# Optimization experiments

Hardware: AMD Instinct MI355X
Metric: run time of the kernel (lower is better)

The kernel has to match this reference:

```python
import jax, jax.numpy as jnp
import numpy as np

NPOINT = 2048
RADIUS = 0.1
NSAMPLE = 32


def fps(xyz, npoint):
    # Furthest point sampling, deterministic start at index 0 (matches pointnet2_utils).
    B, N, _ = xyz.shape
    dist0 = jnp.full((B, N), 1e10, dtype=xyz.dtype)
    far0 = jnp.zeros((B,), dtype=jnp.int32)

    def step(carry, _):
        dist, far = carry
        centroid = jnp.take_along_axis(xyz, far[:, None, None], axis=1)  # (B,1,3)
        d = jnp.sum((xyz - centroid) ** 2, axis=-1)                      # (B,N)
        dist = jnp.minimum(dist, d)
        new_far = jnp.argmax(dist, axis=-1).astype(jnp.int32)
        return (dist, new_far), far

    _, idx = jax.lax.scan(step, (dist0, far0), None, length=npoint)
    return idx.T  # (B, npoint)


def ball_query(xyz, new_xyz, radius, nsample):
    # For each center, indices of up to nsample points within radius (pad with first hit).
    N = xyz.shape[1]
    sqr = jnp.sum((new_xyz[:, :, None, :] - xyz[:, None, :, :]) ** 2, axis=-1)  # (B,S,N)
    cand = jnp.where(sqr <= radius * radius, jnp.arange(N, dtype=jnp.int32), N)
    cand = jnp.sort(cand, axis=-1)[:, :, :nsample]  # (B,S,K)
    first = cand[:, :, :1]
    first = jnp.where(first == N, 0, first)
    return jnp.where(cand == N, first, cand)


def batched_gather(points, idx):
    # points (B,N,C), idx (B,...) -> (B,...,C)
    return jax.vmap(lambda p, i: p[i])(points, idx)


def reference(xyz, features, W0, b0, W1, b1, W2, b2):
    # xyz: (B,N,3), features: (B,C,N)
    fps_idx = fps(xyz, NPOINT)                                  # (B,S)
    new_xyz = batched_gather(xyz, fps_idx)                      # (B,S,3)
    idx = ball_query(xyz, new_xyz, RADIUS, NSAMPLE)             # (B,S,K)

    grouped_xyz = batched_gather(xyz, idx) - new_xyz[:, :, None, :]   # (B,S,K,3) relative coords
    grouped_feat = batched_gather(features.transpose(0, 2, 1), idx)   # (B,S,K,C)
    grouped = jnp.concatenate([grouped_xyz, grouped_feat], axis=-1)   # (B,S,K,C+3)
    x = grouped.transpose(0, 3, 1, 2)                                 # (B,C+3,S,K)

    # SharedMLP: 1x1 conv2d + ReLU stack
    x = jax.nn.relu(jnp.einsum('oi,bisk->bosk', W0, x) + b0[None, :, None, None])
    x = jax.nn.relu(jnp.einsum('oi,bisk->bosk', W1, x) + b1[None, :, None, None])
    x = jax.nn.relu(jnp.einsum('oi,bisk->bosk', W2, x) + b2[None, :, None, None])

    new_features = jnp.max(x, axis=-1)  # max-pool over nsample -> (B,128,S)
    return new_xyz, new_features


def setup_inputs() -> dict:
    key = jax.random.key(0)
    ks = jax.random.split(key, 8)
    B, N, C = 4, 8192, 64
    s = 0.05  # keep activations in a sane range through 3 relu layers
    return {
        'xyz': jax.random.uniform(ks[0], (B, N, 3), dtype=jnp.float32),
        'features': jax.random.normal(ks[1], (B, C, N), dtype=jnp.float32),
        'W0': jax.random.normal(ks[2], (64, 67), dtype=jnp.float32) * s,
        'b0': jax.random.normal(ks[3], (64,), dtype=jnp.float32) * s,
        'W1': jax.random.normal(ks[4], (64, 64), dtype=jnp.float32) * s,
        'b1': jax.random.normal(ks[5], (64,), dtype=jnp.float32) * s,
        'W2': jax.random.normal(ks[6], (128, 64), dtype=jnp.float32) * s,
        'b2': jax.random.normal(ks[7], (128,), dtype=jnp.float32) * s,
    }
```

## Files before the change

### kernel.cpp

```cpp
#include <hip/hip_runtime.h>

#define NB 4
#define NPTS 8192
#define NPOINT 2048
#define NSAMPLE 32
#define CF 64
#define CIN 67
#define G 8

typedef float f32x2 __attribute__((ext_vector_type(2)));
typedef unsigned long long u64;

__device__ __forceinline__ f32x2 pk_add(f32x2 a, f32x2 b) {
  f32x2 d;
  asm("v_pk_add_f32 %0, %1, %2" : "=v"(d) : "v"(a), "v"(b));
  return d;
}
__device__ __forceinline__ f32x2 pk_mul(f32x2 a, f32x2 b) {
  f32x2 d;
  asm("v_pk_mul_f32 %0, %1, %2" : "=v"(d) : "v"(a), "v"(b));
  return d;
}

template <int CTRL, int RM>
__device__ __forceinline__ int dppi(int v) {
  return __builtin_amdgcn_update_dpp(0, v, CTRL, RM, 0xf, true);
}
template <int CTRL, int RM>
__device__ __forceinline__ u64 kstep(u64 k) {
  unsigned lo = (unsigned)k, hi = (unsigned)(k >> 32);
  unsigned olo = (unsigned)dppi<CTRL, RM>((int)lo);
  unsigned ohi = (unsigned)dppi<CTRL, RM>((int)hi);
  u64 o = ((u64)ohi << 32) | olo;
  return o > k ? o : k;
}
__device__ __forceinline__ u64 wave_max_key(u64 key) {
  key = kstep<0x111, 0xf>(key);
  key = kstep<0x112, 0xf>(key);
  key = kstep<0x114, 0xf>(key);
  key = kstep<0x118, 0xf>(key);
  key = kstep<0x142, 0xa>(key);
  key = kstep<0x143, 0xc>(key);
  return key;
}
__device__ __forceinline__ unsigned wave_scan_incl(unsigned v) {
  v += (unsigned)__builtin_amdgcn_update_dpp(0, (int)v, 0x111, 0xf, 0xf, true);
  v += (unsigned)__builtin_amdgcn_update_dpp(0, (int)v, 0x112, 0xf, 0xf, true);
  v += (unsigned)__builtin_amdgcn_update_dpp(0, (int)v, 0x114, 0xf, 0xf, true);
  v += (unsigned)__builtin_amdgcn_update_dpp(0, (int)v, 0x118, 0xf, 0xf, true);
  v += (unsigned)__builtin_amdgcn_update_dpp(0, (int)v, 0x142, 0xa, 0xf, true);
  v += (unsigned)__builtin_amdgcn_update_dpp(0, (int)v, 0x143, 0xc, 0xf, true);
  return v;
}

__device__ __forceinline__ int cell16(float x) {
  int c = (int)(x * 16.0f);
  return c > 15 ? 15 : (c < 0 ? 0 : c);
}
__device__ __forceinline__ unsigned morton12(int ix, int iy, int iz) {
  unsigned m = 0;
#pragma unroll
  for (int k = 0; k < 4; ++k) {
    m |= ((unsigned)((ix >> k) & 1) << (3 * k + 2)) |
         ((unsigned)((iy >> k) & 1) << (3 * k + 1)) |
         ((unsigned)((iz >> k) & 1) << (3 * k + 0));
  }
  return m;
}

__global__ __launch_bounds__(512) void fps_kernel(const float* __restrict__ xyz,
                                                  float* __restrict__ new_xyz) {
  const int b = blockIdx.x;
  const int tid = threadIdx.x;
  const int lane = tid & 63;
  const int wid = tid >> 6;
  __shared__ float sx[NPTS], sy[NPTS], sz[NPTS];
  __shared__ unsigned short sidx16[NPTS];
  __shared__ unsigned offs[4096];
  __shared__ unsigned wsum[8];
  __shared__ int farhist[NPOINT];
  __shared__ __align__(16) u64 skey[2][8];

  const float* xb = xyz + (size_t)b * NPTS * 3;
  for (int i = tid; i < NPTS; i += 512) {
    sx[i] = xb[3 * i + 0];
    sy[i] = xb[3 * i + 1];
    sz[i] = xb[3 * i + 2];
  }
  for (int i = tid; i < 4096; i += 512) offs[i] = 0;
  __syncthreads();
  for (int r = 0; r < 16; ++r) {
    int i = tid + r * 512;
    atomicAdd(&offs[morton12(cell16(sx[i]), cell16(sy[i]), cell16(sz[i]))], 1u);
  }
  __syncthreads();
  unsigned loc[8];
  unsigned s = 0;
#pragma unroll
  for (int q = 0; q < 8; ++q) {
    loc[q] = s;
    s += offs[tid * 8 + q];
  }
  unsigned inc = wave_scan_incl(s);
  if (lane == 63) wsum[wid] = inc;
  __syncthreads();
  unsigned pre = 0;
#pragma unroll
  for (int w = 0; w < 8; ++w) pre += (w < wid) ? wsum[w] : 0u;
  unsigned excl = pre + inc - s;
  __syncthreads();
#pragma unroll
  for (int q = 0; q < 8; ++q) offs[tid * 8 + q] = excl + loc[q];
  __syncthreads();
  for (int r = 0; r < 16; ++r) {
    int i = tid + r * 512;
    unsigned m = morton12(cell16(sx[i]), cell16(sy[i]), cell16(sz[i]));
    unsigned pos = atomicAdd(&offs[m], 1u);
    sidx16[pos] = (unsigned short)i;
  }
  __syncthreads();

  f32x2 px[8], py[8], pz[8];
  float dist[16];
  unsigned noid[16];
  float blx = 1e30f, bhx = -1e30f, bly = 1e30f, bhy = -1e30f,
        blz = 1e30f, bhz = -1e30f;
#pragma unroll
  for (int j = 0; j < 8; ++j) {
    unsigned i0 = sidx16[tid * 16 + 2 * j], i1 = sidx16[tid * 16 + 2 * j + 1];
    noid[2 * j] = ~i0; noid[2 * j + 1] = ~i1;
    float x0 = sx[i0], x1 = sx[i1];
    float y0 = sy[i0], y1 = sy[i1];
    float z0 = sz[i0], z1 = sz[i1];
    px[j].x = x0; px[j].y = x1;
    py[j].x = y0; py[j].y = y1;
    pz[j].x = z0; pz[j].y = z1;
    blx = fminf(blx, fminf(x0, x1)); bhx = fmaxf(bhx, fmaxf(x0, x1));
    bly = fminf(bly, fminf(y0, y1)); bhy = fmaxf(bhy, fmaxf(y0, y1));
    blz = fminf(blz, fminf(z0, z1)); bhz = fmaxf(bhz, fmaxf(z0, z1));
    dist[2 * j] = 1e10f; dist[2 * j + 1] = 1e10f;
  }
  float gmaxd = 1e30f;
  u64 gkey = 0;
  int far = 0;
  for (int it = 0; it < NPOINT; ++it) {
    if (tid == 0) farhist[it] = far;
    const float cx = sx[far], cy = sy[far], cz = sz[far];
    float gx = fmaxf(fmaxf(blx - cx, cx - bhx), 0.f);
    float gy = fmaxf(fmaxf(bly - cy, cy - bhy), 0.f);
    float gz = fmaxf(fmaxf(blz - cz, cz - bhz), 0.f);
    float mind2 = gx * gx + gy * gy + gz * gz;
    if (mind2 * 0.999f < gmaxd) {
      f32x2 ncx, ncy, ncz;
      ncx.x = -cx; ncx.y = -cx;
      ncy.x = -cy; ncy.y = -cy;
      ncz.x = -cz; ncz.y = -cz;
      u64 k = 0;
#pragma unroll
      for (int j = 0; j < 8; ++j) {
        f32x2 dx = pk_add(px[j], ncx);
        f32x2 dy = pk_add(py[j], ncy);
        f32x2 dz = pk_add(pz[j], ncz);
        f32x2 xx = pk_mul(dx, dx);
        f32x2 yy = pk_mul(dy, dy);
        f32x2 dd = pk_add(pk_add(xx, yy), pk_mul(dz, dz));
        float n0 = fminf(dist[2 * j], dd.x);
        float n1 = fminf(dist[2 * j + 1], dd.y);
        dist[2 * j] = n0; dist[2 * j + 1] = n1;
        u64 k0 = ((u64)__float_as_uint(n0) << 32) | noid[2 * j];
        k = k0 > k ? k0 : k;
        u64 k1 = ((u64)__float_as_uint(n1) << 32) | noid[2 * j + 1];
        k = k1 > k ? k1 : k;
      }
      gkey = k;
      gmaxd = __uint_as_float((unsigned)(k >> 32));
    }
    u64 key = wave_max_key(gkey);
    const int p = it & 1;
    if (lane == 63) skey[p][wid] = key;
    __syncthreads();
    const ulonglong2* kp = (const ulonglong2*)&skey[p][0];
    ulonglong2 k0 = kp[0], k1 = kp[1], k2 = kp[2], k3 = kp[3];
    u64 m0 = k0.x > k0.y ? k0.x : k0.y;
    u64 m1 = k1.x > k1.y ? k1.x : k1.y;
    u64 m2 = k2.x > k2.y ? k2.x : k2.y;
    u64 m3 = k3.x > k3.y ? k3.x : k3.y;
    u64 m4 = m0 > m1 ? m0 : m1;
    u64 m5 = m2 > m3 ? m2 : m3;
    u64 best = m4 > m5 ? m4 : m5;
    far = (int)~(unsigned)best;
  }
  __syncthreads();
  for (int t = tid; t < NPOINT; t += 512) {
    int f = farhist[t];
    float* o = new_xyz + ((size_t)b * NPOINT + t) * 3;
    o[0] = sx[f]; o[1] = sy[f]; o[2] = sz[f];
  }
}

__global__ __launch_bounds__(256) void tr_kernel(const float* __restrict__ f,
                                                 float* __restrict__ ft) {
  int idx = blockIdx.x * 256 + threadIdx.x;
  int c = idx & 63;
  int i = (idx >> 6) & (NPTS - 1);
  int b = idx >> 19;
  ft[idx] = f[((size_t)(b * CF + c)) * NPTS + i];
}

__global__ __launch_bounds__(256) void bq_kernel(const float* __restrict__ xyz,
                                                 const float* __restrict__ new_xyz,
                                                 int* __restrict__ idxbuf) {
  const int lane = threadIdx.x & 63;
  const int gw = (blockIdx.x * 256 + threadIdx.x) >> 6;
  const int b = gw >> 11;
  const int j = gw & 2047;
  const float* xb = xyz + (size_t)b * NPTS * 3;
  const float* c = new_xyz + ((size_t)b * NPOINT + j) * 3;
  const float cx = c[0], cy = c[1], cz = c[2];
  int* out = idxbuf + ((size_t)b * NPOINT + j) * NSAMPLE;
  const float r2 = 0.01f;
  int found = 0, first = 0;
  for (int base = 0; base < NPTS && found < NSAMPLE; base += 64) {
    const int i = base + lane;
    float dx = xb[3 * i + 0] - cx, dy = xb[3 * i + 1] - cy, dz = xb[3 * i + 2] - cz;
    float d = __fadd_rn(__fadd_rn(__fmul_rn(dx, dx), __fmul_rn(dy, dy)),
                        __fmul_rn(dz, dz));
    bool in = (d <= r2);
    unsigned long long mask = __ballot(in);
    if (mask) {
      if (found == 0) first = base + (__ffsll(mask) - 1);
      int slot = found + __popcll(mask & ((1ull << lane) - 1ull));
      if (in && slot < NSAMPLE) out[slot] = i;
      found += (int)__popcll(mask);
    }
  }
  for (int s = found + lane; s < NSAMPLE; s += 64) out[s] = first;
}

__global__ __launch_bounds__(256) void mlp_kernel(const float* __restrict__ xyz,
                                                  const float* __restrict__ ft,
                                                  const float* __restrict__ feat,
                                                  const int* __restrict__ idxbuf,
                                                  const float* __restrict__ new_xyz,
                                                  const float* __restrict__ W0,
                                                  const float* __restrict__ b0,
                                                  const float* __restrict__ W1,
                                                  const float* __restrict__ b1,
                                                  const float* __restrict__ W2,
                                                  const float* __restrict__ b2,
                                                  float* __restrict__ out_nf,
                                                  int use_ft) {
  __shared__ __align__(16) float Ws0[CIN * 64];
  __shared__ __align__(16) float Ws1[64 * 64];
  __shared__ __align__(16) float Ws2[64 * 128];
  __shared__ float bs0[64], bs1[64], bs2[128];
  __shared__ __align__(16) float X0[CIN * 32];
  __shared__ __align__(16) float X1[64 * 32];
  const int tid = threadIdx.x;
  const int k = tid & 31;
  const int og = tid >> 5;
  for (int t = tid; t < 64 * CIN; t += 256) {
    int o = t / CIN, c = t - o * CIN;
    Ws0[c * 64 + o] = W0[t];
  }
  for (int t = tid; t < 64 * 64; t += 256) Ws1[(t & 63) * 64 + (t >> 6)] = W1[t];
  for (int t = tid; t < 128 * 64; t += 256) Ws2[(t & 63) * 128 + (t >> 6)] = W2[t];
  if (tid < 64) { bs0[tid] = b0[tid]; bs1[tid] = b1[tid]; }
  if (tid < 128) bs2[tid] = b2[tid];
  __syncthreads();

  for (int g = 0; g < G; ++g) {
    const int cj = blockIdx.x * G + g;
    const int b = cj >> 11;
    const int j = cj & 2047;
    const int ni = idxbuf[cj * NSAMPLE + k];
    if (og == 0) {
      const float* ctr = new_xyz + (size_t)cj * 3;
      const float* pp = xyz + ((size_t)b * NPTS + ni) * 3;
      X0[0 * 32 + k] = pp[0] - ctr[0];
      X0[1 * 32 + k] = pp[1] - ctr[1];
      X0[2 * 32 + k] = pp[2] - ctr[2];
    }
    const int cbase = 3 + og * 8;
    if (use_ft) {
      const float4* fr = (const float4*)(ft + ((size_t)b * NPTS + ni) * CF + og * 8);
      float4 f0 = fr[0], f1 = fr[1];
      X0[(cbase + 0) * 32 + k] = f0.x; X0[(cbase + 1) * 32 + k] = f0.y;
      X0[(cbase + 2) * 32 + k] = f0.z; X0[(cbase + 3) * 32 + k] = f0.w;
      X0[(cbase + 4) * 32 + k] = f1.x; X0[(cbase + 5) * 32 + k] = f1.y;
      X0[(cbase + 6) * 32 + k] = f1.z; X0[(cbase + 7) * 32 + k] = f1.w;
    } else {
      const float* fb = feat + (size_t)b * CF * NPTS + ni;
#pragma unroll
      for (int q = 0; q < 8; ++q)
        X0[(cbase + q) * 32 + k] = fb[(size_t)(og * 8 + q) * NPTS];
    }
    __syncthreads();

    float acc[8];
#pragma unroll
    for (int i = 0; i < 8; ++i) acc[i] = bs0[og * 8 + i];
    for (int c = 0; c < CIN; ++c) {
      float xv = X0[c * 32 + k];
      const float4* wr = (const float4*)&Ws0[c * 64 + og * 8];
      float4 w0 = wr[0], w1 = wr[1];
      acc[0] = fmaf(w0.x, xv, acc[0]); acc[1] = fmaf(w0.y, xv, acc[1]);
      acc[2] = fmaf(w0.z, xv, acc[2]); acc[3] = fmaf(w0.w, xv, acc[3]);
      acc[4] = fmaf(w1.x, xv, acc[4]); acc[5] = fmaf(w1.y, xv, acc[5]);
      acc[6] = fmaf(w1.z, xv, acc[6]); acc[7] = fmaf(w1.w, xv, acc[7]);
    }
#pragma unroll
    for (int i = 0; i < 8; ++i) X1[(og * 8 + i) * 32 + k] = fmaxf(acc[i], 0.f);
    __syncthreads();

    float a1[8];
#pragma unroll
    for (int i = 0; i < 8; ++i) a1[i] = bs1[og * 8 + i];
    for (int c = 0; c < 64; ++c) {
      float xv = X1[c * 32 + k];
      const float4* wr = (const float4*)&Ws1[c * 64 + og * 8];
      float4 w0 = wr[0], w1 = wr[1];
      a1[0] = fmaf(w0.x, xv, a1[0]); a1[1] = fmaf(w0.y, xv, a1[1]);
      a1[2] = fmaf(w0.z, xv, a1[2]); a1[3] = fmaf(w0.w, xv, a1[3]);
      a1[4] = fmaf(w1.x, xv, a1[4]); a1[5] = fmaf(w1.y, xv, a1[5]);
      a1[6] = fmaf(w1.z, xv, a1[6]); a1[7] = fmaf(w1.w, xv, a1[7]);
    }
#pragma unroll
    for (int i = 0; i < 8; ++i) X0[(og * 8 + i) * 32 + k] = fmaxf(a1[i], 0.f);
    __syncthreads();

    float a2[16];
#pragma unroll
    for (int i = 0; i < 16; ++i) a2[i] = bs2[og * 16 + i];
    for (int c = 0; c < 64; ++c) {
      float xv = X0[c * 32 + k];
      const float4* wr = (const float4*)&Ws2[c * 128 + og * 16];
      float4 w0 = wr[0], w1 = wr[1], w2 = wr[2], w3 = wr[3];
      a2[0]  = fmaf(w0.x, xv, a2[0]);  a2[1]  = fmaf(w0.y, xv, a2[1]);
      a2[2]  = fmaf(w0.z, xv, a2[2]);  a2[3]  = fmaf(w0.w, xv, a2[3]);
      a2[4]  = fmaf(w1.x, xv, a2[4]);  a2[5]  = fmaf(w1.y, xv, a2[5]);
      a2[6]  = fmaf(w1.z, xv, a2[6]);  a2[7]  = fmaf(w1.w, xv, a2[7]);
      a2[8]  = fmaf(w2.x, xv, a2[8]);  a2[9]  = fmaf(w2.y, xv, a2[9]);
      a2[10] = fmaf(w2.z, xv, a2[10]); a2[11] = fmaf(w2.w, xv, a2[11]);
      a2[12] = fmaf(w3.x, xv, a2[12]); a2[13] = fmaf(w3.y, xv, a2[13]);
      a2[14] = fmaf(w3.z, xv, a2[14]); a2[15] = fmaf(w3.w, xv, a2[15]);
    }
#pragma unroll
    for (int i = 0; i < 16; ++i) {
      float v = fmaxf(a2[i], 0.f);
#pragma unroll
      for (int m = 1; m < 32; m <<= 1) v = fmaxf(v, __shfl_xor(v, m));
      a2[i] = v;
    }
    if (k == 0) {
#pragma unroll
      for (int i = 0; i < 16; ++i)
        out_nf[((size_t)b * 128 + og * 16 + i) * NPOINT + j] = a2[i];
    }
    __syncthreads();
  }
}

extern "C" void kernel_launch(void* const* d_in, const int* in_sizes, int n_in,
                              void* d_out, int out_size, void* d_ws, size_t ws_size,
                              hipStream_t stream) {
  (void)in_sizes; (void)n_in; (void)out_size;
  const float* xyz  = (const float*)d_in[0];
  const float* feat = (const float*)d_in[1];
  const float* W0   = (const float*)d_in[2];
  const float* b0   = (const float*)d_in[3];
  const float* W1   = (const float*)d_in[4];
  const float* b1   = (const float*)d_in[5];
  const float* W2   = (const float*)d_in[6];
  const float* b2   = (const float*)d_in[7];
  float* new_xyz = (float*)d_out;
  float* out_nf  = (float*)d_out + (size_t)NB * NPOINT * 3;

  int* idxbuf = (int*)d_ws;
  size_t idx_bytes = (size_t)NB * NPOINT * NSAMPLE * sizeof(int);
  float* ft = (float*)((char*)d_ws + idx_bytes);
  size_t need = idx_bytes + (size_t)NB * NPTS * CF * sizeof(float);
  int use_ft = (ws_size >= need) ? 1 : 0;

  fps_kernel<<<NB, 512, 0, stream>>>(xyz, new_xyz);
  if (use_ft) tr_kernel<<<(NB * NPTS * CF) / 256, 256, 0, stream>>>(feat, ft);
  bq_kernel<<<(NB * NPOINT) / 4, 256, 0, stream>>>(xyz, new_xyz, idxbuf);
  mlp_kernel<<<(NB * NPOINT) / G, 256, 0, stream>>>(xyz, ft, feat, idxbuf, new_xyz,
                                                    W0, b0, W1, b1, W2, b2,
                                                    out_nf, use_ft);
}
```

Measured before the change: 2.124 ms.

## Halve FPS block size with two bbox-culled subgroups per thread and f64 key max

The FPS kernel now runs 256 threads instead of 512. Each thread holds two 16-point subgroups, each with its own bounding box, and a subgroup's update is skipped when no lane in the wave needs it (ballot). The packed 64-bit argmax keys are compared as doubles with fmax instead of integer compares, which works because both halves are non-negative and order the same way. This targets the per-iteration barrier and the cross-wave reduction cost in the serial 2048-step loop, at the price of more registers per thread and less parallel slack.

```diff
diff --git a/kernel.cpp b/kernel.cpp
--- a/kernel.cpp
+++ b/kernel.cpp
@@ -26,21 +26,26 @@
 __device__ __forceinline__ int dppi(int v) {
   return __builtin_amdgcn_update_dpp(0, v, CTRL, RM, 0xf, true);
 }
+__device__ __forceinline__ double kmax(double a, double b) { return fmax(a, b); }
+__device__ __forceinline__ double mkkey(unsigned hi, unsigned lo) {
+  return __longlong_as_double(((long long)hi << 32) | lo);
+}
 template <int CTRL, int RM>
-__device__ __forceinline__ u64 kstep(u64 k) {
-  unsigned lo = (unsigned)k, hi = (unsigned)(k >> 32);
+__device__ __forceinline__ double kstep_d(double k) {
+  long long bb = __double_as_longlong(k);
+  unsigned lo = (unsigned)bb, hi = (unsigned)(bb >> 32);
   unsigned olo = (unsigned)dppi<CTRL, RM>((int)lo);
   unsigned ohi = (unsigned)dppi<CTRL, RM>((int)hi);
-  u64 o = ((u64)ohi << 32) | olo;
-  return o > k ? o : k;
-}
-__device__ __forceinline__ u64 wave_max_key(u64 key) {
-  key = kstep<0x111, 0xf>(key);
-  key = kstep<0x112, 0xf>(key);
-  key = kstep<0x114, 0xf>(key);
-  key = kstep<0x118, 0xf>(key);
-  key = kstep<0x142, 0xa>(key);
-  key = kstep<0x143, 0xc>(key);
+  double o = __longlong_as_double(((long long)ohi << 32) | olo);
+  return fmax(k, o);
+}
+__device__ __forceinline__ double wave_max_key_d(double key) {
+  key = kstep_d<0x111, 0xf>(key);
+  key = kstep_d<0x112, 0xf>(key);
+  key = kstep_d<0x114, 0xf>(key);
+  key = kstep_d<0x118, 0xf>(key);
+  key = kstep_d<0x142, 0xa>(key);
+  key = kstep_d<0x143, 0xc>(key);
   return key;
 }
 __device__ __forceinline__ unsigned wave_scan_incl(unsigned v) {
@@ -68,7 +73,72 @@
   return m;
 }
 
-__global__ __launch_bounds__(512) void fps_kernel(const float* __restrict__ xyz,
+struct SubGrp {
+  f32x2 px[8], py[8], pz[8];
+  float dist[16];
+  unsigned noid[16];
+  float blx, bhx, bly, bhy, blz, bhz;
+  double skey;
+  float gmaxd;
+
+  __device__ __forceinline__ void load(const unsigned short* sidx16,
+                                       const float* sx, const float* sy,
+                                       const float* sz, int base) {
+    blx = 1e30f; bhx = -1e30f; bly = 1e30f; bhy = -1e30f;
+    blz = 1e30f; bhz = -1e30f;
+#pragma unroll
+    for (int j = 0; j < 8; ++j) {
+      unsigned i0 = sidx16[base + 2 * j], i1 = sidx16[base + 2 * j + 1];
+      noid[2 * j] = ~i0; noid[2 * j + 1] = ~i1;
+      float x0 = sx[i0], x1 = sx[i1];
+      float y0 = sy[i0], y1 = sy[i1];
+      float z0 = sz[i0], z1 = sz[i1];
+      px[j].x = x0; px[j].y = x1;
+      py[j].x = y0; py[j].y = y1;
+      pz[j].x = z0; pz[j].y = z1;
+      blx = fminf(blx, fminf(x0, x1)); bhx = fmaxf(bhx, fmaxf(x0, x1));
+      bly = fminf(bly, fminf(y0, y1)); bhy = fmaxf(bhy, fmaxf(y0, y1));
+      blz = fminf(blz, fminf(z0, z1)); bhz = fmaxf(bhz, fmaxf(z0, z1));
+      dist[2 * j] = 1e10f; dist[2 * j + 1] = 1e10f;
+    }
+    skey = 0.0;
+    gmaxd = 1e30f;
+  }
+
+  __device__ __forceinline__ bool dirty(float cx, float cy, float cz) const {
+    float gx = fmaxf(fmaxf(blx - cx, cx - bhx), 0.f);
+    float gy = fmaxf(fmaxf(bly - cy, cy - bhy), 0.f);
+    float gz = fmaxf(fmaxf(blz - cz, cz - bhz), 0.f);
+    float mind2 = gx * gx + gy * gy + gz * gz;
+    return mind2 * 0.999f < gmaxd;
+  }
+
+  __device__ __forceinline__ void update(float cx, float cy, float cz) {
+    f32x2 ncx, ncy, ncz;
+    ncx.x = -cx; ncx.y = -cx;
+    ncy.x = -cy; ncy.y = -cy;
+    ncz.x = -cz; ncz.y = -cz;
+    double k = 0.0;
+#pragma unroll
+    for (int j = 0; j < 8; ++j) {
+      f32x2 dx = pk_add(px[j], ncx);
+      f32x2 dy = pk_add(py[j], ncy);
+      f32x2 dz = pk_add(pz[j], ncz);
+      f32x2 xx = pk_mul(dx, dx);
+      f32x2 yy = pk_mul(dy, dy);
+      f32x2 dd = pk_add(pk_add(xx, yy), pk_mul(dz, dz));
+      float n0 = fminf(dist[2 * j], dd.x);
+      float n1 = fminf(dist[2 * j + 1], dd.y);
+      dist[2 * j] = n0; dist[2 * j + 1] = n1;
+      k = kmax(k, mkkey(__float_as_uint(n0), noid[2 * j]));
+      k = kmax(k, mkkey(__float_as_uint(n1), noid[2 * j + 1]));
+    }
+    skey = k;
+    gmaxd = __uint_as_float((unsigned)((u64)__double_as_longlong(k) >> 32));
+  }
+};
+
+__global__ __launch_bounds__(256) void fps_kernel(const float* __restrict__ xyz,
                                                   float* __restrict__ new_xyz) {
   const int b = blockIdx.x;
   const int tid = threadIdx.x;
@@ -77,121 +147,76 @@
   __shared__ float sx[NPTS], sy[NPTS], sz[NPTS];
   __shared__ unsigned short sidx16[NPTS];
   __shared__ unsigned offs[4096];
-  __shared__ unsigned wsum[8];
+  __shared__ unsigned wsum[4];
   __shared__ int farhist[NPOINT];
-  __shared__ __align__(16) u64 skey[2][8];
+  __shared__ __align__(16) double skey[2][4];
 
   const float* xb = xyz + (size_t)b * NPTS * 3;
-  for (int i = tid; i < NPTS; i += 512) {
+  for (int i = tid; i < NPTS; i += 256) {
     sx[i] = xb[3 * i + 0];
     sy[i] = xb[3 * i + 1];
     sz[i] = xb[3 * i + 2];
   }
-  for (int i = tid; i < 4096; i += 512) offs[i] = 0;
-  __syncthreads();
-  for (int r = 0; r < 16; ++r) {
-    int i = tid + r * 512;
+  for (int i = tid; i < 4096; i += 256) offs[i] = 0;
+  __syncthreads();
+  for (int r = 0; r < 32; ++r) {
+    int i = tid + r * 256;
     atomicAdd(&offs[morton12(cell16(sx[i]), cell16(sy[i]), cell16(sz[i]))], 1u);
   }
   __syncthreads();
-  unsigned loc[8];
+  unsigned loc[16];
   unsigned s = 0;
 #pragma unroll
-  for (int q = 0; q < 8; ++q) {
+  for (int q = 0; q < 16; ++q) {
     loc[q] = s;
-    s += offs[tid * 8 + q];
+    s += offs[tid * 16 + q];
   }
   unsigned inc = wave_scan_incl(s);
   if (lane == 63) wsum[wid] = inc;
   __syncthreads();
   unsigned pre = 0;
 #pragma unroll
-  for (int w = 0; w < 8; ++w) pre += (w < wid) ? wsum[w] : 0u;
+  for (int w = 0; w < 4; ++w) pre += (w < wid) ? wsum[w] : 0u;
   unsigned excl = pre + inc - s;
   __syncthreads();
 #pragma unroll
-  for (int q = 0; q < 8; ++q) offs[tid * 8 + q] = excl + loc[q];
-  __syncthreads();
-  for (int r = 0; r < 16; ++r) {
-    int i = tid + r * 512;
+  for (int q = 0; q < 16; ++q) offs[tid * 16 + q] = excl + loc[q];
+  __syncthreads();
+  for (int r = 0; r < 32; ++r) {
+    int i = tid + r * 256;
     unsigned m = morton12(cell16(sx[i]), cell16(sy[i]), cell16(sz[i]));
     unsigned pos = atomicAdd(&offs[m], 1u);
     sidx16[pos] = (unsigned short)i;
   }
   __syncthreads();
 
-  f32x2 px[8], py[8], pz[8];
-  float dist[16];
-  unsigned noid[16];
-  float blx = 1e30f, bhx = -1e30f, bly = 1e30f, bhy = -1e30f,
-        blz = 1e30f, bhz = -1e30f;
-#pragma unroll
-  for (int j = 0; j < 8; ++j) {
-    unsigned i0 = sidx16[tid * 16 + 2 * j], i1 = sidx16[tid * 16 + 2 * j + 1];
-    noid[2 * j] = ~i0; noid[2 * j + 1] = ~i1;
-    float x0 = sx[i0], x1 = sx[i1];
-    float y0 = sy[i0], y1 = sy[i1];
-    float z0 = sz[i0], z1 = sz[i1];
-    px[j].x = x0; px[j].y = x1;
-    py[j].x = y0; py[j].y = y1;
-    pz[j].x = z0; pz[j].y = z1;
-    blx = fminf(blx, fminf(x0, x1)); bhx = fmaxf(bhx, fmaxf(x0, x1));
-    bly = fminf(bly, fminf(y0, y1)); bhy = fmaxf(bhy, fmaxf(y0, y1));
-    blz = fminf(blz, fminf(z0, z1)); bhz = fmaxf(bhz, fmaxf(z0, z1));
-    dist[2 * j] = 1e10f; dist[2 * j + 1] = 1e10f;
-  }
-  float gmaxd = 1e30f;
-  u64 gkey = 0;
+  SubGrp A, B;
+  A.load(sidx16, sx, sy, sz, tid * 32);
+  B.load(sidx16, sx, sy, sz, tid * 32 + 16);
+
   int far = 0;
   for (int it = 0; it < NPOINT; ++it) {
     if (tid == 0) farhist[it] = far;
     const float cx = sx[far], cy = sy[far], cz = sz[far];
-    float gx = fmaxf(fmaxf(blx - cx, cx - bhx), 0.f);
-    float gy = fmaxf(fmaxf(bly - cy, cy - bhy), 0.f);
-    float gz = fmaxf(fmaxf(blz - cz, cz - bhz), 0.f);
-    float mind2 = gx * gx + gy * gy + gz * gz;
-    if (mind2 * 0.999f < gmaxd) {
-      f32x2 ncx, ncy, ncz;
-      ncx.x = -cx; ncx.y = -cx;
-      ncy.x = -cy; ncy.y = -cy;
-      ncz.x = -cz; ncz.y = -cz;
-      u64 k = 0;
-#pragma unroll
-      for (int j = 0; j < 8; ++j) {
-        f32x2 dx = pk_add(px[j], ncx);
-        f32x2 dy = pk_add(py[j], ncy);
-        f32x2 dz = pk_add(pz[j], ncz);
-        f32x2 xx = pk_mul(dx, dx);
-        f32x2 yy = pk_mul(dy, dy);
-        f32x2 dd = pk_add(pk_add(xx, yy), pk_mul(dz, dz));
-        float n0 = fminf(dist[2 * j], dd.x);
-        float n1 = fminf(dist[2 * j + 1], dd.y);
-        dist[2 * j] = n0; dist[2 * j + 1] = n1;
-        u64 k0 = ((u64)__float_as_uint(n0) << 32) | noid[2 * j];
-        k = k0 > k ? k0 : k;
-        u64 k1 = ((u64)__float_as_uint(n1) << 32) | noid[2 * j + 1];
-        k = k1 > k ? k1 : k;
-      }
-      gkey = k;
-      gmaxd = __uint_as_float((unsigned)(k >> 32));
-    }
-    u64 key = wave_max_key(gkey);
+    bool da = A.dirty(cx, cy, cz);
+    if (__ballot(da)) {
+      if (da) A.update(cx, cy, cz);
+    }
+    bool db = B.dirty(cx, cy, cz);
+    if (__ballot(db)) {
+      if (db) B.update(cx, cy, cz);
+    }
+    double key = wave_max_key_d(kmax(A.skey, B.skey));
     const int p = it & 1;
     if (lane == 63) skey[p][wid] = key;
     __syncthreads();
-    const ulonglong2* kp = (const ulonglong2*)&skey[p][0];
-    ulonglong2 k0 = kp[0], k1 = kp[1], k2 = kp[2], k3 = kp[3];
-    u64 m0 = k0.x > k0.y ? k0.x : k0.y;
-    u64 m1 = k1.x > k1.y ? k1.x : k1.y;
-    u64 m2 = k2.x > k2.y ? k2.x : k2.y;
-    u64 m3 = k3.x > k3.y ? k3.x : k3.y;
-    u64 m4 = m0 > m1 ? m0 : m1;
-    u64 m5 = m2 > m3 ? m2 : m3;
-    u64 best = m4 > m5 ? m4 : m5;
-    far = (int)~(unsigned)best;
-  }
-  __syncthreads();
-  for (int t = tid; t < NPOINT; t += 512) {
+    const double2* kp = (const double2*)&skey[p][0];
+    double2 a0 = kp[0], a1 = kp[1];
+    double best = kmax(kmax(a0.x, a0.y), kmax(a1.x, a1.y));
+    far = (int)~(unsigned)(u64)__double_as_longlong(best);
+  }
+  __syncthreads();
+  for (int t = tid; t < NPOINT; t += 256) {
     int f = farhist[t];
     float* o = new_xyz + ((size_t)b * NPOINT + t) * 3;
     o[0] = sx[f]; o[1] = sy[f]; o[2] = sz[f];
@@ -382,7 +407,7 @@
   size_t need = idx_bytes + (size_t)NB * NPTS * CF * sizeof(float);
   int use_ft = (ws_size >= need) ? 1 : 0;
 
-  fps_kernel<<<NB, 512, 0, stream>>>(xyz, new_xyz);
+  fps_kernel<<<NB, 256, 0, stream>>>(xyz, new_xyz);
   if (use_ft) tr_kernel<<<(NB * NPTS * CF) / 256, 256, 0, stream>>>(feat, ft);
   bq_kernel<<<(NB * NPOINT) / 4, 256, 0, stream>>>(xyz, new_xyz, idxbuf);
   mlp_kernel<<<(NB * NPOINT) / G, 256, 0, stream>>>(xyz, ft, feat, idxbuf, new_xyz,
```

New measurement: 2.570 ms. +21.0%, slower.
